# Performance work log

Measured on AMD Instinct MI355X. Metric: run time of the kernel, lower is better.

Reference implementation:

```python
import jax, jax.numpy as jnp
import numpy as np
from jax import lax

NUM_TAGS = 48
BATCH = 512
SEQ_LEN = 1024


def setup_inputs() -> dict:
    key = jax.random.key(0)
    k1, k2, k3, k4 = jax.random.split(key, 4)
    emissions = jax.random.normal(k1, (BATCH, SEQ_LEN, NUM_TAGS), dtype=jnp.float32)
    mask = jnp.ones((BATCH, SEQ_LEN), dtype=jnp.int32)
    transitions = jax.random.normal(k2, (NUM_TAGS, NUM_TAGS), dtype=jnp.float32)
    start_transitions = jax.random.normal(k3, (NUM_TAGS,), dtype=jnp.float32)
    end_transitions = jax.random.normal(k4, (NUM_TAGS,), dtype=jnp.float32)
    return {
        "emissions": emissions,
        "mask": mask,
        "transitions": transitions,
        "start_transitions": start_transitions,
        "end_transitions": end_transitions,
    }


def reference(emissions, mask, transitions, start_transitions, end_transitions):
    """Viterbi decode. mask is accepted but unused, matching the original module."""
    # emissions: [B, S, T]
    init_scores = start_transitions + emissions[:, 0]  # [B, T]

    def step(scores, em_t):
        # scores: [B, T] best score ending in each prev tag
        scores_with_trans = scores[:, :, None] + transitions  # [B, Tprev, Tcur]
        idx = jnp.argmax(scores_with_trans, axis=1)            # [B, T] backpointers
        new_scores = jnp.max(scores_with_trans, axis=1) + em_t  # [B, T]
        return new_scores, idx

    # scan over timesteps 1..S-1 (time-major emissions)
    em_rest = jnp.swapaxes(emissions[:, 1:], 0, 1)  # [S-1, B, T]
    scores, backptrs = lax.scan(step, init_scores, em_rest)  # backptrs: [S-1, B, T]

    scores = scores + end_transitions
    best_tags = jnp.argmax(scores, axis=1)  # [B] tag at position S-1

    def backtrace(tag, bp_t):
        # tag: [B] tag at position t+1; bp_t: [B, T] backpointers into position t
        prev = jnp.take_along_axis(bp_t, tag[:, None], axis=1)[:, 0]
        return prev, tag  # emit tag at position t+1

    first_tag, tags_rest = lax.scan(backtrace, best_tags, backptrs, reverse=True)
    # tags_rest[i] = tag at position i+1, shape [S-1, B]
    best_paths = jnp.concatenate(
        [first_tag[:, None], jnp.swapaxes(tags_rest, 0, 1)], axis=1
    )  # [B, S]
    return best_paths
```

## Files before the change

### kernel.cpp

```cpp
#include <hip/hip_runtime.h>

#define NTAG 48
#define SEQ 1024
#define NBATCH 512
#define CH 128
#define NCH (SEQ / CH)
#define CHF (CH * NTAG)
#define NISS (CHF * 4 / 1024)
#define NEG_INF (-3.402823466e+38f)

__device__ __forceinline__ float rl_f32(float v, int lane) {
    return __int_as_float(__builtin_amdgcn_readlane(__float_as_int(v), lane));
}

__device__ __forceinline__ float max3(float a, float b, float c) {
    float d;
    asm("v_max3_f32 %0, %1, %2, %3" : "=v"(d) : "v"(a), "v"(b), "v"(c));
    return d;
}

#define GLDS16(gp, lp)                                                                   \
    __builtin_amdgcn_global_load_lds((const __attribute__((address_space(1))) void*)(gp),\
                                     (__attribute__((address_space(3))) void*)(lp),      \
                                     16, 0, 0)

__global__ __launch_bounds__(64, 1) void crf_viterbi_kernel(
    const float* __restrict__ em,
    const float* __restrict__ trans,
    const float* __restrict__ start,
    const float* __restrict__ endt,
    int* __restrict__ out,
    unsigned char* __restrict__ bp)
{
    const int b  = blockIdx.x;
    const int j  = threadIdx.x;
    const int jj = (j < NTAG) ? j : (NTAG - 1);

    __shared__ float stage[2][CHF];
    __shared__ int obuf[SEQ];

    float trg[NTAG];
#pragma unroll
    for (int i = 0; i < NTAG; ++i) trg[i] = trans[i * NTAG + jj];

    const float* emb = em + (size_t)b * SEQ * NTAG;
    unsigned char* bpb = bp + (size_t)b * SEQ * NTAG;

#pragma unroll
    for (int k = 0; k < NISS; ++k)
        GLDS16(emb + k * 256 + j * 4, &stage[0][k * 256]);
    asm volatile("s_waitcnt vmcnt(0)" ::: "memory");

    float score = start[jj] + stage[0][jj];

    int cb = 0;
    for (int c = 0; c < NCH; ++c) {
        if (c + 1 < NCH) {
            const float* gs = emb + (size_t)(c + 1) * CHF;
#pragma unroll
            for (int k = 0; k < NISS; ++k)
                GLDS16(gs + k * 256 + j * 4, &stage[cb ^ 1][k * 256]);
        }
        const int tt0 = (c == 0) ? 1 : 0;
        for (int tt = tt0; tt < CH; ++tt) {
            float em_j = stage[cb][tt * NTAG + jj];

            float cand[NTAG];
#pragma unroll
            for (int i = 0; i < NTAG; ++i)
                cand[i] = rl_f32(score, i) + trg[i];

            float l1[16];
#pragma unroll
            for (int k = 0; k < 16; ++k)
                l1[k] = max3(cand[3 * k], cand[3 * k + 1], cand[3 * k + 2]);
            float l2[6];
            l2[0] = max3(l1[0],  l1[1],  l1[2]);
            l2[1] = max3(l1[3],  l1[4],  l1[5]);
            l2[2] = max3(l1[6],  l1[7],  l1[8]);
            l2[3] = max3(l1[9],  l1[10], l1[11]);
            l2[4] = max3(l1[12], l1[13], l1[14]);
            l2[5] = l1[15];
            float m0 = max3(l2[0], l2[1], l2[2]);
            float m1 = max3(l2[3], l2[4], l2[5]);
            float best = fmaxf(m0, m1);

            int pi = 0;
#pragma unroll
            for (int i = NTAG - 1; i >= 0; --i)
                pi = (cand[i] == best) ? i : pi;

            int t = c * CH + tt;
            if (j < NTAG) bpb[(size_t)t * NTAG + j] = (unsigned char)pi;
            score = best + em_j;
        }
        asm volatile("s_waitcnt vmcnt(0)" ::: "memory");
        cb ^= 1;
    }

    float fs = (j < NTAG) ? (score + endt[jj]) : NEG_INF;
    float mx = fs;
    mx = fmaxf(mx, __shfl_xor(mx, 32, 64));
    mx = fmaxf(mx, __shfl_xor(mx, 16, 64));
    mx = fmaxf(mx, __shfl_xor(mx,  8, 64));
    mx = fmaxf(mx, __shfl_xor(mx,  4, 64));
    mx = fmaxf(mx, __shfl_xor(mx,  2, 64));
    mx = fmaxf(mx, __shfl_xor(mx,  1, 64));
    unsigned long long bl = __ballot(fs == mx);
    int tag = __ffsll(bl) - 1;

    if (j == 0) obuf[SEQ - 1] = tag;

    int cur[16], nxt[16];
    int t = SEQ - 1;
    int n = 16;
#pragma unroll
    for (int k = 0; k < 16; ++k)
        cur[k] = (int)bpb[(size_t)(t - k) * NTAG + jj];

    while (t >= 1) {
        int t2 = t - n;
        int n2 = 0;
        if (t2 >= 1) {
            n2 = (t2 >= 16) ? 16 : t2;
#pragma unroll
            for (int k = 0; k < 16; ++k)
                if (k < n2) nxt[k] = (int)bpb[(size_t)(t2 - k) * NTAG + jj];
        }
#pragma unroll
        for (int k = 0; k < 16; ++k) {
            if (k < n) {
                tag = __builtin_amdgcn_readlane(cur[k], tag);
                if (j == 0) obuf[t - k - 1] = tag;
            }
        }
#pragma unroll
        for (int k = 0; k < 16; ++k) cur[k] = nxt[k];
        t = t2; n = n2;
    }

    __syncthreads();

    int* outb = out + (size_t)b * SEQ;
#pragma unroll
    for (int t0 = 0; t0 < SEQ / 64; ++t0)
        outb[t0 * 64 + j] = obuf[t0 * 64 + j];
}

extern "C" void kernel_launch(void* const* d_in, const int* in_sizes, int n_in,
                              void* d_out, int out_size, void* d_ws, size_t ws_size,
                              hipStream_t stream) {
    const float* em    = (const float*)d_in[0];
    const float* trans = (const float*)d_in[2];
    const float* start = (const float*)d_in[3];
    const float* endt  = (const float*)d_in[4];
    int* out = (int*)d_out;
    unsigned char* bpw = (unsigned char*)d_ws;

    crf_viterbi_kernel<<<NBATCH, 64, 0, stream>>>(em, trans, start, endt, out, bpw);
}
```

Baseline: 1.024 ms.

## Split Viterbi max-reduction over previous tags across four wavefronts

Each block now runs four wavefronts. Each wavefront handles a quarter (12) of the previous-tag candidates and writes its partial max and argmax to shared memory. After a barrier, every wave combines the four partials, and the backpointer store rotates among the waves. This cuts the per-step serial readlane/max chain from 48 candidates to 12, at the cost of one LDS round trip and a workgroup barrier on every timestep. The emission staging loads and the output copy are redistributed over 256 threads.

```diff
diff --git a/kernel.cpp b/kernel.cpp
--- a/kernel.cpp
+++ b/kernel.cpp
@@ -6,7 +6,8 @@
 #define CH 128
 #define NCH (SEQ / CH)
 #define CHF (CH * NTAG)
-#define NISS (CHF * 4 / 1024)
+#define NISS (CHF / 1024)
+#define QW 12
 #define NEG_INF (-3.402823466e+38f)
 
 __device__ __forceinline__ float rl_f32(float v, int lane) {
@@ -24,7 +25,19 @@
                                      (__attribute__((address_space(3))) void*)(lp),      \
                                      16, 0, 0)
 
-__global__ __launch_bounds__(64, 1) void crf_viterbi_kernel(
+#define BAR_LGKM() do {                                            \
+    asm volatile("s_waitcnt lgkmcnt(0)" ::: "memory");             \
+    __builtin_amdgcn_s_barrier();                                  \
+    asm volatile("" ::: "memory");                                 \
+} while (0)
+
+#define BAR_ALL() do {                                             \
+    asm volatile("s_waitcnt vmcnt(0) lgkmcnt(0)" ::: "memory");    \
+    __builtin_amdgcn_s_barrier();                                  \
+    asm volatile("" ::: "memory");                                 \
+} while (0)
+
+__global__ __launch_bounds__(256, 1) void crf_viterbi_kernel(
     const float* __restrict__ em,
     const float* __restrict__ trans,
     const float* __restrict__ start,
@@ -32,119 +45,137 @@
     int* __restrict__ out,
     unsigned char* __restrict__ bp)
 {
-    const int b  = blockIdx.x;
-    const int j  = threadIdx.x;
-    const int jj = (j < NTAG) ? j : (NTAG - 1);
+    const int b     = blockIdx.x;
+    const int tid   = threadIdx.x;
+    const int w     = tid >> 6;
+    const int j     = tid & 63;
+    const int jj    = (j < NTAG) ? j : (NTAG - 1);
+    const int wbase = w * QW;
 
     __shared__ float stage[2][CHF];
-    __shared__ int obuf[SEQ];
+    __shared__ float pval[2][4][NTAG];
+    __shared__ int   pidx[2][4][NTAG];
+    __shared__ int   obuf[SEQ];
 
-    float trg[NTAG];
+    float trgq[QW];
 #pragma unroll
-    for (int i = 0; i < NTAG; ++i) trg[i] = trans[i * NTAG + jj];
+    for (int k = 0; k < QW; ++k) trgq[k] = trans[(wbase + k) * NTAG + jj];
 
     const float* emb = em + (size_t)b * SEQ * NTAG;
     unsigned char* bpb = bp + (size_t)b * SEQ * NTAG;
 
 #pragma unroll
     for (int k = 0; k < NISS; ++k)
-        GLDS16(emb + k * 256 + j * 4, &stage[0][k * 256]);
-    asm volatile("s_waitcnt vmcnt(0)" ::: "memory");
+        GLDS16(emb + k * 1024 + tid * 4, &stage[0][k * 1024 + (w << 8)]);
+    BAR_ALL();
 
     float score = start[jj] + stage[0][jj];
 
-    int cb = 0;
+    int cb = 0, pb = 0;
     for (int c = 0; c < NCH; ++c) {
         if (c + 1 < NCH) {
             const float* gs = emb + (size_t)(c + 1) * CHF;
 #pragma unroll
             for (int k = 0; k < NISS; ++k)
-                GLDS16(gs + k * 256 + j * 4, &stage[cb ^ 1][k * 256]);
+                GLDS16(gs + k * 1024 + tid * 4, &stage[cb ^ 1][k * 1024 + (w << 8)]);
         }
         const int tt0 = (c == 0) ? 1 : 0;
         for (int tt = tt0; tt < CH; ++tt) {
             float em_j = stage[cb][tt * NTAG + jj];
 
-            float cand[NTAG];
+            float cd[QW];
 #pragma unroll
-            for (int i = 0; i < NTAG; ++i)
-                cand[i] = rl_f32(score, i) + trg[i];
+            for (int i = 0; i < QW; ++i)
+                cd[i] = rl_f32(score, wbase + i) + trgq[i];
 
-            float l1[16];
+            float m0 = max3(cd[0], cd[1],  cd[2]);
+            float m1 = max3(cd[3], cd[4],  cd[5]);
+            float m2 = max3(cd[6], cd[7],  cd[8]);
+            float m3 = max3(cd[9], cd[10], cd[11]);
+            float qv = fmaxf(max3(m0, m1, m2), m3);
+
+            int qi = 0;
 #pragma unroll
-            for (int k = 0; k < 16; ++k)
-                l1[k] = max3(cand[3 * k], cand[3 * k + 1], cand[3 * k + 2]);
-            float l2[6];
-            l2[0] = max3(l1[0],  l1[1],  l1[2]);
-            l2[1] = max3(l1[3],  l1[4],  l1[5]);
-            l2[2] = max3(l1[6],  l1[7],  l1[8]);
-            l2[3] = max3(l1[9],  l1[10], l1[11]);
-            l2[4] = max3(l1[12], l1[13], l1[14]);
-            l2[5] = l1[15];
-            float m0 = max3(l2[0], l2[1], l2[2]);
-            float m1 = max3(l2[3], l2[4], l2[5]);
-            float best = fmaxf(m0, m1);
+            for (int i = QW - 1; i >= 0; --i)
+                qi = (cd[i] == qv) ? i : qi;
 
-            int pi = 0;
-#pragma unroll
-            for (int i = NTAG - 1; i >= 0; --i)
-                pi = (cand[i] == best) ? i : pi;
+            if (j < NTAG) {
+                pval[pb][w][j] = qv;
+                pidx[pb][w][j] = wbase + qi;
+            }
+            BAR_LGKM();
 
-            int t = c * CH + tt;
-            if (j < NTAG) bpb[(size_t)t * NTAG + j] = (unsigned char)pi;
+            float q0 = pval[pb][0][jj];
+            float q1 = pval[pb][1][jj];
+            float q2 = pval[pb][2][jj];
+            float q3 = pval[pb][3][jj];
+            float best = fmaxf(fmaxf(q0, q1), fmaxf(q2, q3));
+
+            if (w == (tt & 3) && j < NTAG) {
+                int i0 = pidx[pb][0][j], i1 = pidx[pb][1][j];
+                int i2 = pidx[pb][2][j], i3 = pidx[pb][3][j];
+                int pi = (q0 == best) ? i0
+                       : (q1 == best) ? i1
+                       : (q2 == best) ? i2 : i3;
+                int t = c * CH + tt;
+                bpb[(size_t)t * NTAG + j] = (unsigned char)pi;
+            }
             score = best + em_j;
+            pb ^= 1;
         }
-        asm volatile("s_waitcnt vmcnt(0)" ::: "memory");
+        BAR_ALL();
         cb ^= 1;
     }
 
-    float fs = (j < NTAG) ? (score + endt[jj]) : NEG_INF;
-    float mx = fs;
-    mx = fmaxf(mx, __shfl_xor(mx, 32, 64));
-    mx = fmaxf(mx, __shfl_xor(mx, 16, 64));
-    mx = fmaxf(mx, __shfl_xor(mx,  8, 64));
-    mx = fmaxf(mx, __shfl_xor(mx,  4, 64));
-    mx = fmaxf(mx, __shfl_xor(mx,  2, 64));
-    mx = fmaxf(mx, __shfl_xor(mx,  1, 64));
-    unsigned long long bl = __ballot(fs == mx);
-    int tag = __ffsll(bl) - 1;
+    if (w == 0) {
+        float fs = (j < NTAG) ? (score + endt[jj]) : NEG_INF;
+        float mx = fs;
+        mx = fmaxf(mx, __shfl_xor(mx, 32, 64));
+        mx = fmaxf(mx, __shfl_xor(mx, 16, 64));
+        mx = fmaxf(mx, __shfl_xor(mx,  8, 64));
+        mx = fmaxf(mx, __shfl_xor(mx,  4, 64));
+        mx = fmaxf(mx, __shfl_xor(mx,  2, 64));
+        mx = fmaxf(mx, __shfl_xor(mx,  1, 64));
+        unsigned long long bl = __ballot(fs == mx);
+        int tag = __ffsll(bl) - 1;
 
-    if (j == 0) obuf[SEQ - 1] = tag;
+        if (j == 0) obuf[SEQ - 1] = tag;
 
-    int cur[16], nxt[16];
-    int t = SEQ - 1;
-    int n = 16;
+        int cur[16], nxt[16];
+        int t = SEQ - 1;
+        int n = 16;
 #pragma unroll
-    for (int k = 0; k < 16; ++k)
-        cur[k] = (int)bpb[(size_t)(t - k) * NTAG + jj];
+        for (int k = 0; k < 16; ++k)
+            cur[k] = (int)bpb[(size_t)(t - k) * NTAG + jj];
 
-    while (t >= 1) {
-        int t2 = t - n;
-        int n2 = 0;
-        if (t2 >= 1) {
-            n2 = (t2 >= 16) ? 16 : t2;
+        while (t >= 1) {
+            int t2 = t - n;
+            int n2 = 0;
+            if (t2 >= 1) {
+                n2 = (t2 >= 16) ? 16 : t2;
 #pragma unroll
-            for (int k = 0; k < 16; ++k)
-                if (k < n2) nxt[k] = (int)bpb[(size_t)(t2 - k) * NTAG + jj];
+                for (int k = 0; k < 16; ++k)
+                    if (k < n2) nxt[k] = (int)bpb[(size_t)(t2 - k) * NTAG + jj];
+            }
+#pragma unroll
+            for (int k = 0; k < 16; ++k) {
+                if (k < n) {
+                    tag = __builtin_amdgcn_readlane(cur[k], tag);
+                    if (j == 0) obuf[t - k - 1] = tag;
+                }
+            }
+#pragma unroll
+            for (int k = 0; k < 16; ++k) cur[k] = nxt[k];
+            t = t2; n = n2;
         }
-#pragma unroll
-        for (int k = 0; k < 16; ++k) {
-            if (k < n) {
-                tag = __builtin_amdgcn_readlane(cur[k], tag);
-                if (j == 0) obuf[t - k - 1] = tag;
-            }
-        }
-#pragma unroll
-        for (int k = 0; k < 16; ++k) cur[k] = nxt[k];
-        t = t2; n = n2;
     }
 
     __syncthreads();
 
     int* outb = out + (size_t)b * SEQ;
 #pragma unroll
-    for (int t0 = 0; t0 < SEQ / 64; ++t0)
-        outb[t0 * 64 + j] = obuf[t0 * 64 + j];
+    for (int k = 0; k < SEQ / 256; ++k)
+        outb[k * 256 + tid] = obuf[k * 256 + tid];
 }
 
 extern "C" void kernel_launch(void* const* d_in, const int* in_sizes, int n_in,
@@ -157,5 +188,5 @@
     int* out = (int*)d_out;
     unsigned char* bpw = (unsigned char*)d_ws;
 
-    crf_viterbi_kernel<<<NBATCH, 64, 0, stream>>>(em, trans, start, endt, out, bpw);
+    crf_viterbi_kernel<<<NBATCH, 256, 0, stream>>>(em, trans, start, endt, out, bpw);
 }
```

Result: faster. 830.3 us (-18.9%).
